# Optimization experiments

Measured on AMD Instinct MI355X. Metric: run time of the kernel, lower is better.

## Reference

```python
import jax, jax.numpy as jnp
import numpy as np

B, N, M, K = 4, 16384, 16384, 16   # batch, points, centers, neighbors
C, O, G = 64, 64, 8                # in_planes, out_planes, group


def setup_inputs() -> dict:
    key = jax.random.key(0)
    ks = jax.random.split(key, 16)
    r = lambda i, sh, s=1.0: jax.random.normal(ks[i], sh, jnp.float32) * s
    return dict(
        center_pos=r(0, (B, M, 3)),
        center_fea=r(1, (B, C, M)),
        pos=r(2, (B, N, 3)),
        fea=r(3, (B, C, N)),
        idx=jax.random.randint(ks[4], (B, M, K), 0, N, jnp.int32),
        # linear q/k/v
        Wq=r(5, (C, O), 0.05), bq=jnp.zeros((O,), jnp.float32),
        Wk=r(6, (C, O), 0.05), bk=jnp.zeros((O,), jnp.float32),
        Wv=r(7, (C, O), 0.05), bv=jnp.zeros((O,), jnp.float32),
        # center_pos_encode: conv1x1(3->O, no bias) + folded BN (scale,shift) + relu + conv1x1(O->O)
        cpe_w1=r(8, (3, O), 0.05), cpe_s=jnp.ones((O,), jnp.float32), cpe_b=jnp.zeros((O,), jnp.float32),
        cpe_w2=r(9, (O, O), 0.05), cpe_b2=jnp.zeros((O,), jnp.float32),
        # pos_encode (Conv2d 1x1 == per-point linear)
        pe_w1=r(10, (3, O), 0.05), pe_s=jnp.ones((O,), jnp.float32), pe_b=jnp.zeros((O,), jnp.float32),
        pe_w2=r(11, (O, O), 0.05), pe_b2=jnp.zeros((O,), jnp.float32),
        # weight_encode (O -> G)
        we_w1=r(12, (O, G), 0.05), we_s=jnp.ones((G,), jnp.float32), we_b=jnp.zeros((G,), jnp.float32),
        we_w2=r(13, (G, G), 0.05), we_b2=jnp.zeros((G,), jnp.float32),
    )


def _mlp2(x, w1, s, b, w2, b2):
    # conv1x1(no bias) -> inference BatchNorm folded to (scale, shift) -> ReLU -> conv1x1(+bias)
    h = jax.nn.relu(x @ w1 * s + b)
    return h @ w2 + b2


def reference(center_pos, center_fea, pos, fea, idx,
              Wq, bq, Wk, bk, Wv, bv,
              cpe_w1, cpe_s, cpe_b, cpe_w2, cpe_b2,
              pe_w1, pe_s, pe_b, pe_w2, pe_b2,
              we_w1, we_s, we_b, we_w2, we_b2):
    x_q = center_fea.transpose(0, 2, 1) @ Wq + bq        # [B,M,O]
    ft = fea.transpose(0, 2, 1)                          # [B,N,C]
    x_k = ft @ Wk + bk                                   # [B,N,O]
    x_v = ft @ Wv + bv                                   # [B,N,O]

    gather = jax.vmap(lambda a, i: a[i])                 # per-batch irregular gather
    nk = gather(x_k, idx)                                # [B,M,K,O]
    nv = gather(x_v, idx)                                # [B,M,K,O]
    npos = gather(pos, idx) - center_pos[:, :, None, :]  # [B,M,K,3] relative coords

    cpr = _mlp2(center_pos, cpe_w1, cpe_s, cpe_b, cpe_w2, cpe_b2)  # [B,M,O]
    pr = _mlp2(npos, pe_w1, pe_s, pe_b, pe_w2, pe_b2)              # [B,M,K,O]

    r_qk = nk - x_q[:, :, None, :] + cpr[:, :, None, :]  # [B,M,K,O]
    v = nv + pr                                          # [B,M,K,O]

    w = _mlp2(r_qk, we_w1, we_s, we_b, we_w2, we_b2)     # [B,M,K,G]
    w = jax.nn.softmax(w, axis=2)                        # softmax over neighbors

    v = v.reshape(B, M, K, G, O // G)
    out = jnp.einsum('bmkgi,bmkg->bmgi', v, w).reshape(B, M, O)
    return out.transpose(0, 2, 1)                        # [B,O,M]
```

## Files before the change

### kernel.cpp

```cpp
#include <hip/hip_runtime.h>
#include <hip/hip_bf16.h>

typedef unsigned short u16;
typedef __attribute__((ext_vector_type(8))) __bf16 bf8v;
typedef __attribute__((ext_vector_type(8))) _Float16 f16x8;
typedef __attribute__((ext_vector_type(2))) _Float16 h2v;
typedef __attribute__((ext_vector_type(4))) float f32x4;
typedef __attribute__((ext_vector_type(4))) unsigned uint4v;
typedef __attribute__((ext_vector_type(4))) int int4v;

#define B_ 4
#define N_ 16384
#define M_ 16384
#define K_ 16
#define C_ 64
#define O_ 64
#define G_ 8

__device__ __forceinline__ float bf2f(u16 x){
  union { unsigned u; float f; } v; v.u = ((unsigned)x) << 16; return v.f;
}
__device__ __forceinline__ u16 f2bf(float f){
  union { float f; unsigned u; } v; v.f = f;
  unsigned u = v.u;
  return (u16)((u + 0x7FFFu + ((u >> 16) & 1u)) >> 16);
}
__device__ __forceinline__ u16 f2h(float f){
  union { _Float16 h; u16 u; } v; v.h = (_Float16)f; return v.u;
}
__device__ __forceinline__ h2v mkh2(float a, float b){
  h2v r = {(_Float16)a, (_Float16)b}; return r;
}

__global__ __launch_bounds__(256) void pre_kernel(
    const float* __restrict__ center_pos, const float* __restrict__ center_fea,
    const float* __restrict__ pos, const float* __restrict__ fea,
    const float* __restrict__ Wq, const float* __restrict__ bq,
    const float* __restrict__ Wk, const float* __restrict__ bk,
    const float* __restrict__ Wv, const float* __restrict__ bv,
    const float* __restrict__ cpe_w1, const float* __restrict__ cpe_s, const float* __restrict__ cpe_b,
    const float* __restrict__ cpe_w2, const float* __restrict__ cpe_b2,
    const float* __restrict__ we_w1,
    u16* __restrict__ xk, u16* __restrict__ xv, float* __restrict__ qw,
    float* __restrict__ pos4, float* __restrict__ cp4)
{
  __shared__ u16 sWT[128*72];
  __shared__ u16 sA[64*72];
  __shared__ u16 sOut[64*136];
  __shared__ float sMisc[256];
  __shared__ float sCi[8];
  int tid = threadIdx.x;
  int l = tid & 63, w = tid >> 6, c = l & 15, q = l >> 4;
  int blk = blockIdx.x;

  if (blk < 256){
    int P0 = blk * 256; int b = P0 >> 14; int n00 = P0 & (N_-1);
    const float* fb = fea + (long)b*C_*N_;
    for (int e = tid; e < 8192; e += 256){
      int k = e >> 7, col = e & 127;
      float v = (col < 64) ? Wk[k*64 + col] : Wv[k*64 + (col-64)];
      sWT[col*72 + k] = f2bf(v);
    }
    if (tid < 128) sMisc[tid] = (tid < 64) ? bk[tid] : bv[tid-64];
    {
      long pg = (long)P0 + tid;
      f32x4 r = {pos[pg*3], pos[pg*3+1], pos[pg*3+2], 0.f};
      ((f32x4*)pos4)[pg] = r;
    }

    #pragma unroll 1
    for (int s = 0; s < 4; s++){
      int n0 = n00 + s*64;
      #pragma unroll
      for (int pp = 0; pp < 4; pp++){
        int k = pp*16 + (tid >> 4);
        int nf = (tid & 15)*4;
        f32x4 v = *(const f32x4*)&fb[(long)k*N_ + n0 + nf];
        sA[(nf+0)*72+k] = f2bf(v[0]); sA[(nf+1)*72+k] = f2bf(v[1]);
        sA[(nf+2)*72+k] = f2bf(v[2]); sA[(nf+3)*72+k] = f2bf(v[3]);
      }
      __syncthreads();

      bf8v af0 = *(const bf8v*)&sA[(w*16+c)*72 + q*8];
      bf8v af1 = *(const bf8v*)&sA[(w*16+c)*72 + 32 + q*8];
      f32x4 acc[8];
      #pragma unroll
      for (int t = 0; t < 8; t++){
        float bb = sMisc[16*t + c];
        f32x4 a_ = {bb, bb, bb, bb};
        bf8v b0 = *(const bf8v*)&sWT[(16*t + c)*72 + q*8];
        bf8v b1 = *(const bf8v*)&sWT[(16*t + c)*72 + 32 + q*8];
        a_ = __builtin_amdgcn_mfma_f32_16x16x32_bf16(af0, b0, a_, 0,0,0);
        a_ = __builtin_amdgcn_mfma_f32_16x16x32_bf16(af1, b1, a_, 0,0,0);
        acc[t] = a_;
      }
      #pragma unroll
      for (int t = 0; t < 8; t++)
        #pragma unroll
        for (int r = 0; r < 4; r++)
          sOut[(w*16 + q*4 + r)*136 + 16*t + c] = f2bf(acc[t][r]);
      __syncthreads();

      #pragma unroll
      for (int rep = 0; rep < 4; rep++){
        int chunk = rep*256 + tid;
        int pt = chunk >> 4, c8i = chunk & 15;
        uint4v val = *(const uint4v*)&sOut[pt*136 + c8i*8];
        int col8 = c8i*8;
        long row = (long)P0 + s*64 + pt;
        if (col8 < 64) *(uint4v*)(xk + row*64 + col8)      = val;
        else           *(uint4v*)(xv + row*64 + (col8-64)) = val;
      }
      __syncthreads();
    }
  } else {
    int P0 = (blk - 256) * 256; int b = P0 >> 14; int m00 = P0 & (M_-1);
    const float* cfb = center_fea + (long)b*C_*M_;
    float* sWe = (float*)sOut;
    float* sQ  = (float*)sOut;
    for (int e = tid; e < 512; e += 256) sWe[e] = we_w1[e];
    if (tid < 64){
      float sc = cpe_s[tid];
      sMisc[tid]     = cpe_w1[tid]*sc;
      sMisc[64+tid]  = cpe_w1[64+tid]*sc;
      sMisc[128+tid] = cpe_w1[128+tid]*sc;
      sMisc[192+tid] = cpe_b[tid];
    }
    {
      long pg = (long)P0 + tid;
      f32x4 r = {center_pos[pg*3], center_pos[pg*3+1], center_pos[pg*3+2], 0.f};
      ((f32x4*)cp4)[pg] = r;
    }
    __syncthreads();
    {
      int k = tid >> 1, g0 = (tid & 1)*4;
      const float* brow = (k < 64) ? (cpe_w2 + k*64) : (Wq + (k-64)*64);
      float sgn = (k < 64) ? 1.f : -1.f;
      float aw[4] = {0.f,0.f,0.f,0.f};
      for (int o = 0; o < 64; o++){
        float bo = brow[o]*sgn;
        #pragma unroll
        for (int gg=0; gg<4; gg++) aw[gg] += bo * sWe[o*8 + g0+gg];
      }
      #pragma unroll
      for (int gg=0; gg<4; gg++) sWT[(g0+gg)*136 + k] = f2bf(aw[gg]);
    }
    for (int e = tid; e < 2176; e += 256){
      int r = e / 136, cc = e % 136;
      if (r >= 8 || cc >= 128) sWT[e] = 0;
    }
    if (tid < 8){
      float s = 0.f;
      for (int o = 0; o < 64; o++) s += (cpe_b2[o] - bq[o]) * sWe[o*8 + tid];
      sCi[tid] = s;
    }
    __syncthreads();

    #pragma unroll 1
    for (int s = 0; s < 4; s++){
      int m0 = m00 + s*64;
      #pragma unroll
      for (int pp = 0; pp < 4; pp++){
        int k = pp*16 + (tid >> 4);
        int nf = (tid & 15)*4;
        f32x4 v = *(const f32x4*)&cfb[(long)k*M_ + m0 + nf];
        sA[(nf+0)*72+k] = f2bf(v[0]); sA[(nf+1)*72+k] = f2bf(v[1]);
        sA[(nf+2)*72+k] = f2bf(v[2]); sA[(nf+3)*72+k] = f2bf(v[3]);
      }
      long c3 = (long)(P0 + s*64 + w*16 + c)*3;
      float cp0 = center_pos[c3], cp1 = center_pos[c3+1], cp2 = center_pos[c3+2];
      __syncthreads();

      bf8v ah[2];
      #pragma unroll
      for (int ks = 0; ks < 2; ks++){
        union { bf8v v; u16 sv[8]; } ua;
        #pragma unroll
        for (int j = 0; j < 8; j++){
          int h = ks*32 + q*8 + j;
          float hv = cp0*sMisc[h] + cp1*sMisc[64+h] + cp2*sMisc[128+h] + sMisc[192+h];
          ua.sv[j] = f2bf(fmaxf(hv, 0.f));
        }
        ah[ks] = ua.v;
      }
      bf8v acf0 = *(const bf8v*)&sA[(w*16+c)*72 + q*8];
      bf8v acf1 = *(const bf8v*)&sA[(w*16+c)*72 + 32 + q*8];

      float ci = (c < 8) ? sCi[c] : 0.f;
      f32x4 aq = {ci, ci, ci, ci};
      {
        bf8v b0 = *(const bf8v*)&sWT[c*136 + q*8];
        bf8v b1 = *(const bf8v*)&sWT[c*136 + 32 + q*8];
        bf8v b2 = *(const bf8v*)&sWT[c*136 + 64 + q*8];
        bf8v b3 = *(const bf8v*)&sWT[c*136 + 96 + q*8];
        aq = __builtin_amdgcn_mfma_f32_16x16x32_bf16(ah[0], b0, aq, 0,0,0);
        aq = __builtin_amdgcn_mfma_f32_16x16x32_bf16(ah[1], b1, aq, 0,0,0);
        aq = __builtin_amdgcn_mfma_f32_16x16x32_bf16(acf0,  b2, aq, 0,0,0);
        aq = __builtin_amdgcn_mfma_f32_16x16x32_bf16(acf1,  b3, aq, 0,0,0);
      }
      __syncthreads();
      if (c < 8){
        #pragma unroll
        for (int r = 0; r < 4; r++) sQ[(w*16 + q*4 + r)*8 + c] = aq[r];
      }
      __syncthreads();
      for (int e = tid; e < 512; e += 256)
        qw[(long)(P0 + s*64)*8 + e] = sQ[e];
      __syncthreads();
    }
  }
}

__global__ __launch_bounds__(256) void attn_kernel(
    const float* __restrict__ cp4, const float* __restrict__ pos4,
    const int* __restrict__ idx,
    const float* __restrict__ pe_w1, const float* __restrict__ pe_s, const float* __restrict__ pe_b,
    const float* __restrict__ pe_w2, const float* __restrict__ pe_b2,
    const float* __restrict__ we_w1, const float* __restrict__ we_s, const float* __restrict__ we_b,
    const float* __restrict__ we_w2, const float* __restrict__ we_b2,
    const u16* __restrict__ xk, const u16* __restrict__ xv, const float* __restrict__ qw,
    float* __restrict__ out)
{
  int tid = threadIdx.x;
  __shared__ float s_w1f[192], s_pb[64], s_pb2[64], s_ww2[64];
  __shared__ float s_ws8[8], s_wb8[8], s_wb28[8];
  __shared__ f32x4 s_dyn4[720];
  __shared__ float s_tile[64*66];

  char* dynb = (char*)s_dyn4;

  if (tid < 64){
    float sc = pe_s[tid];
    s_w1f[tid]     = pe_w1[tid]*sc;
    s_w1f[64+tid]  = pe_w1[64+tid]*sc;
    s_w1f[128+tid] = pe_w1[128+tid]*sc;
    s_pb[tid]  = pe_b[tid];
    s_pb2[tid] = pe_b2[tid];
    s_ww2[tid] = we_w2[tid];
  }
  if (tid >= 64 && tid < 72){
    int g = tid-64;
    s_ws8[g]=we_s[g]; s_wb8[g]=we_b[g]; s_wb28[g]=we_b2[g];
  }
  u16* stg = (u16*)dynb;
  #pragma unroll
  for (int pp = 0; pp < 4; pp++){
    int row = pp*16 + (tid >> 4);
    int colf = (tid & 15)*4;
    f32x4 v = *(const f32x4*)&pe_w2[row*64 + colf];
    stg[(colf+0)*72+row] = f2h(v[0]); stg[(colf+1)*72+row] = f2h(v[1]);
    stg[(colf+2)*72+row] = f2h(v[2]); stg[(colf+3)*72+row] = f2h(v[3]);
  }
  u16* stg2 = (u16*)(dynb + 9216);
  for (int e = tid; e < 512; e += 256){
    int k = e >> 3, cc = e & 7;
    stg2[cc*72 + k] = f2bf(we_w1[e]);
  }
  for (int e = tid; e < 576; e += 256) stg2[576 + e] = 0;
  __syncthreads();

  int w = tid >> 6, l = tid & 63, c = l & 15, q = l >> 4, c8 = c & 7;

  f16x8 pw2f[4][2];
  bf8v ww1f[2];
  f16x8 w2B, hz8;
  #pragma unroll
  for (int t = 0; t < 4; t++){
    pw2f[t][0] = *(const f16x8*)&stg[(t*16+c)*72 + q*8];
    pw2f[t][1] = *(const f16x8*)&stg[(t*16+c)*72 + 32 + q*8];
  }
  ww1f[0] = *(const bf8v*)&stg2[c*72 + q*8];
  ww1f[1] = *(const bf8v*)&stg2[c*72 + 32 + q*8];
  {
    union { f16x8 v; u16 s[8]; } uu;
    #pragma unroll
    for (int j = 0; j < 8; j++)
      uu.s[j] = (q == 0 && c < 8) ? f2h(s_ww2[j*8 + c]) : (u16)0;
    w2B = uu.v;
    #pragma unroll
    for (int j = 0; j < 8; j++) uu.s[j] = 0;
    hz8 = uu.v;
  }
  h2v cw0[2][4], cw1[2][4], cw2[2][4], cb[2][4];
  #pragma unroll
  for (int ks = 0; ks < 2; ks++)
    #pragma unroll
    for (int jj = 0; jj < 4; jj++){
      int o = ks*32 + q*8 + jj*2;
      cw0[ks][jj] = mkh2(s_w1f[o],     s_w1f[o+1]);
      cw1[ks][jj] = mkh2(s_w1f[64+o],  s_w1f[65+o]);
      cw2[ks][jj] = mkh2(s_w1f[128+o], s_w1f[129+o]);
      cb [ks][jj] = mkh2(s_pb[o],      s_pb[o+1]);
    }
  int qok = (q < 2);
  int gq = (q & 1)*4;
  float wsr0 = qok ? s_ws8[gq+0] : 0.f, wbr0 = qok ? s_wb8[gq+0] : 0.f;
  float wsr1 = qok ? s_ws8[gq+1] : 0.f, wbr1 = qok ? s_wb8[gq+1] : 0.f;
  float wsr2 = qok ? s_ws8[gq+2] : 0.f, wbr2 = qok ? s_wb8[gq+2] : 0.f;
  float wsr3 = qok ? s_ws8[gq+3] : 0.f, wbr3 = qok ? s_wb8[gq+3] : 0.f;
  float wb2_c = s_wb28[c8];
  float pb2l = s_pb2[l];
  h2v hz2 = {(_Float16)0.f, (_Float16)0.f};
  __syncthreads();

  float* swt0 = (float*)(dynb + w*1536);
  float* swt1 = swt0 + 192;

  int blk = blockIdx.x;
  int pbase = (((blk & 7) << 7) | (blk >> 3)) * 64;
  int b = pbase >> 14;
  const u16* xkb = xk + (long)b * N_ * 64;
  const u16* xvb = xv + (long)b * N_ * 64;
  const f32x4* pos4b = ((const f32x4*)pos4) + (long)b * N_;
  int ch = c >> 3;

  int pb0 = pbase + w*16;
  const int*   idxl = idx + (long)pb0*16 + c;
  const int*   idxq = idx + (long)pb0*16 + q*4;
  const f32x4* qwl4 = ((const f32x4*)(qw + (long)pb0*8)) + (q & 1);
  const f32x4* cp4l = ((const f32x4*)cp4) + pb0;

  auto hidden_sm = [&](bf8v k0, bf8v k1, f32x4 qv, float* swtp){
    f32x4 h2t = {qv[0], qv[1], qv[2], qv[3]};
    h2t = __builtin_amdgcn_mfma_f32_16x16x32_bf16(ww1f[0], k0, h2t, 0,0,0);
    h2t = __builtin_amdgcn_mfma_f32_16x16x32_bf16(ww1f[1], k1, h2t, 0,0,0);
    h2v hp01 = mkh2(fmaxf(h2t[0]*wsr0 + wbr0, 0.f), fmaxf(h2t[1]*wsr1 + wbr1, 0.f));
    h2v hp23 = mkh2(fmaxf(h2t[2]*wsr2 + wbr2, 0.f), fmaxf(h2t[3]*wsr3 + wbr3, 0.f));
    union { h2v h; int i; } u01, u23, x01, x23;
    u01.h = hp01; u23.h = hp23;
    x01.i = __shfl_xor(u01.i, 16, 64);
    x23.i = __shfl_xor(u23.i, 16, 64);
    f16x8 ahf;
    {
      union { f16x8 v; h2v p[4]; } au;
      au.p[0] = u01.h; au.p[1] = u23.h; au.p[2] = x01.h; au.p[3] = x23.h;
      ahf = (q == 0) ? au.v : hz8;
    }
    f32x4 wlv = {wb2_c, wb2_c, wb2_c, wb2_c};
    wlv = __builtin_amdgcn_mfma_f32_16x16x32_f16(ahf, w2B, wlv, 0,0,0);
    float e0 = exp2f(wlv[0]*1.44269504f);
    float e1 = exp2f(wlv[1]*1.44269504f);
    float e2 = exp2f(wlv[2]*1.44269504f);
    float e3 = exp2f(wlv[3]*1.44269504f);
    float sm = e0+e1+e2+e3;
    sm += __shfl_xor(sm, 16, 64);
    sm += __shfl_xor(sm, 32, 64);
    float rn = 1.0f / sm;
    if (c < 8){
      f32x4 ev = {e0*rn, e1*rn, e2*rn, e3*rn};
      *(f32x4*)&swtp[c*20 + q*4] = ev;
    }
  };

  struct H1 { f16x8 a, b; };
  auto make_h1 = [&](float n0, float n1, float n2){
    h2v n0h = {(_Float16)n0, (_Float16)n0};
    h2v n1h = {(_Float16)n1, (_Float16)n1};
    h2v n2h = {(_Float16)n2, (_Float16)n2};
    H1 o;
    #pragma unroll
    for (int ks = 0; ks < 2; ks++){
      union { f16x8 v; h2v p[4]; } hu;
      #pragma unroll
      for (int jj = 0; jj < 4; jj++){
        h2v a = cb[ks][jj];
        a = n0h*cw0[ks][jj] + a;
        a = n1h*cw1[ks][jj] + a;
        a = n2h*cw2[ks][jj] + a;
        hu.p[jj] = __builtin_elementwise_max(a, hz2);
      }
      if (ks == 0) o.a = hu.v; else o.b = hu.v;
    }
    return o;
  };

  auto finish = [&](H1 h, unsigned (&vv)[4][4],
                    f32x4 wv0, f32x4 wv1, f32x4 wv2, f32x4 wv3, int row){
    float ov[4];
    #pragma unroll
    for (int t = 0; t < 4; t++){
      f32x4 z = {bf2f((u16)vv[0][t]), bf2f((u16)vv[1][t]),
                 bf2f((u16)vv[2][t]), bf2f((u16)vv[3][t])};
      z = __builtin_amdgcn_mfma_f32_16x16x32_f16(h.a, pw2f[t][0], z, 0,0,0);
      z = __builtin_amdgcn_mfma_f32_16x16x32_f16(h.b, pw2f[t][1], z, 0,0,0);
      f32x4 wv = (t==0) ? wv0 : (t==1) ? wv1 : (t==2) ? wv2 : wv3;
      ov[t] = z[0]*wv[0] + z[1]*wv[1] + z[2]*wv[2] + z[3]*wv[3];
    }
    int hi2 = (q & 2);
    float s0 = hi2 ? ov[0] : ov[2];
    float s1 = hi2 ? ov[1] : ov[3];
    float m0 = hi2 ? ov[2] : ov[0];
    float m1 = hi2 ? ov[3] : ov[1];
    float u_ = m0 + __shfl_xor(s0, 32, 64);
    float v_ = m1 + __shfl_xor(s1, 32, 64);
    float s2 = (q & 1) ? u_ : v_;
    float m2 = (q & 1) ? v_ : u_;
    float ovsel = m2 + __shfl_xor(s2, 16, 64);
    s_tile[row*66 + l] = ovsel + pb2l;
  };

  int j0 = idxl[0];
  int j1 = idxl[16];
  int ivE = idxl[32];
  int ivO = idxl[48];
  f32x4 qvP = qwl4[0];
  f32x4 qvO = qwl4[2];
  f32x4 qvE = qwl4[4];
  f32x4 cpE = cp4l[0], cpO = cp4l[1];
  f32x4 ppE = pos4b[j0], ppO = pos4b[j1];
  const u16* krP = xkb + (size_t)j0*64;
  bf8v kP0 = *(const bf8v*)(krP + q*8);
  bf8v kP1 = *(const bf8v*)(krP + 32 + q*8);
  const u16* kr1 = xkb + (size_t)j1*64;
  bf8v kO0 = *(const bf8v*)(kr1 + q*8);
  bf8v kO1 = *(const bf8v*)(kr1 + 32 + q*8);
  int4v iq0 = *(const int4v*)&idxq[0];
  int4v iqO = *(const int4v*)&idxq[16];
  int4v iqE = *(const int4v*)&idxq[32];
  unsigned vcE[4][4];
  #pragma unroll
  for (int r = 0; r < 4; r++){
    const u16* vr = xvb + (size_t)iq0[r]*64 + c;
    #pragma unroll
    for (int t = 0; t < 4; t++) vcE[r][t] = vr[t*16];
  }
  hidden_sm(kP0, kP1, qvP, swt0);

  #pragma unroll 1
  for (int ii = 0; ii < 8; ii++){
    int i0 = 2*ii, i1 = i0 + 1;

    f32x4 wa0 = *(const f32x4*)&swt0[(0*2+ch)*20 + q*4];
    f32x4 wa1 = *(const f32x4*)&swt0[(1*2+ch)*20 + q*4];
    f32x4 wa2 = *(const f32x4*)&swt0[(2*2+ch)*20 + q*4];
    f32x4 wa3 = *(const f32x4*)&swt0[(3*2+ch)*20 + q*4];
    float na0 = ppE[0]-cpE[0], na1 = ppE[1]-cpE[1], na2 = ppE[2]-cpE[2];
    const u16* krE = xkb + (size_t)ivE*64;
    bf8v kE20 = *(const bf8v*)(krE + q*8);
    bf8v kE21 = *(const bf8v*)(krE + 32 + q*8);
    ppE = pos4b[ivE];
    cpE = cp4l[(i0+2 <= 15) ? i0+2 : 15];
    unsigned vcO[4][4];
    #pragma unroll
    for (int r = 0; r < 4; r++){
      const u16* vr = xvb + (size_t)iqO[r]*64 + c;
      #pragma unroll
      for (int t = 0; t < 4; t++) vcO[r][t] = vr[t*16];
    }
    iqO = *(const int4v*)&idxq[((i0+3 <= 15) ? i0+3 : 15)*16];
    ivE = idxl[((i0+4 <= 15) ? i0+4 : 15)*16];
    hidden_sm(kO0, kO1, qvO, swt1);
    qvO = qwl4[((i0+3 <= 15) ? i0+3 : 15)*2];
    H1 hE = make_h1(na0, na1, na2);
    finish(hE, vcE, wa0, wa1, wa2, wa3, w*16 + i0);

    f32x4 wb0 = *(const f32x4*)&swt1[(0*2+ch)*20 + q*4];
    f32x4 wb1 = *(const f32x4*)&swt1[(1*2+ch)*20 + q*4];
    f32x4 wb2 = *(const f32x4*)&swt1[(2*2+ch)*20 + q*4];
    f32x4 wb3 = *(const f32x4*)&swt1[(3*2+ch)*20 + q*4];
    float nb0 = ppO[0]-cpO[0], nb1 = ppO[1]-cpO[1], nb2 = ppO[2]-cpO[2];
    const u16* krO = xkb + (size_t)ivO*64;
    kO0 = *(const bf8v*)(krO + q*8);
    kO1 = *(const bf8v*)(krO + 32 + q*8);
    ppO = pos4b[ivO];
    cpO = cp4l[(i0+3 <= 15) ? i0+3 : 15];
    #pragma unroll
    for (int r = 0; r < 4; r++){
      const u16* vr = xvb + (size_t)iqE[r]*64 + c;
      #pragma unroll
      for (int t = 0; t < 4; t++) vcE[r][t] = vr[t*16];
    }
    iqE = *(const int4v*)&idxq[((i0+4 <= 15) ? i0+4 : 15)*16];
    ivO = idxl[((i0+5 <= 15) ? i0+5 : 15)*16];
    if (ii < 7)
      hidden_sm(kE20, kE21, qvE, swt0);
    qvE = qwl4[((i0+4 <= 15) ? i0+4 : 15)*2];
    H1 hO = make_h1(nb0, nb1, nb2);
    finish(hO, vcO, wb0, wb1, wb2, wb3, w*16 + i1);
  }
  __syncthreads();

  {
    int o0 = tid >> 5, pt0 = tid & 31;
    int m0 = pbase & (M_-1);
    #pragma unroll
    for (int half = 0; half < 2; half++){
      int pt = pt0 + half*32;
      long outb = ((long)b*64) * M_ + m0 + pt;
      #pragma unroll
      for (int ii = 0; ii < 8; ii++){
        int o = o0*8 + ii;
        out[outb + (long)o*M_] = s_tile[pt*66 + o];
      }
    }
  }
}

extern "C" void kernel_launch(void* const* d_in, const int* in_sizes, int n_in,
                              void* d_out, int out_size, void* d_ws, size_t ws_size,
                              hipStream_t stream) {
  const float* center_pos = (const float*)d_in[0];
  const float* center_fea = (const float*)d_in[1];
  const float* pos        = (const float*)d_in[2];
  const float* fea        = (const float*)d_in[3];
  const int*   idx        = (const int*)d_in[4];
  const float* Wq = (const float*)d_in[5];   const float* bq = (const float*)d_in[6];
  const float* Wk = (const float*)d_in[7];   const float* bk = (const float*)d_in[8];
  const float* Wv = (const float*)d_in[9];   const float* bv = (const float*)d_in[10];
  const float* cpe_w1 = (const float*)d_in[11]; const float* cpe_s = (const float*)d_in[12];
  const float* cpe_b  = (const float*)d_in[13]; const float* cpe_w2 = (const float*)d_in[14];
  const float* cpe_b2 = (const float*)d_in[15];
  const float* pe_w1 = (const float*)d_in[16]; const float* pe_s = (const float*)d_in[17];
  const float* pe_b  = (const float*)d_in[18]; const float* pe_w2 = (const float*)d_in[19];
  const float* pe_b2 = (const float*)d_in[20];
  const float* we_w1 = (const float*)d_in[21]; const float* we_s = (const float*)d_in[22];
  const float* we_b  = (const float*)d_in[23]; const float* we_w2 = (const float*)d_in[24];
  const float* we_b2 = (const float*)d_in[25];

  const size_t SZ = (size_t)B_*N_*64;
  u16* xk = (u16*)d_ws;
  u16* xv = xk + SZ;
  float* qwp = (float*)(xv + SZ);
  float* pos4p = qwp + (size_t)B_*M_*8;
  float* cp4p  = pos4p + (size_t)B_*N_*4;
  float* outp = (float*)d_out;

  hipLaunchKernelGGL(pre_kernel, dim3(512), dim3(256), 0, stream,
      center_pos, center_fea, pos, fea, Wq, bq, Wk, bk, Wv, bv,
      cpe_w1, cpe_s, cpe_b, cpe_w2, cpe_b2, we_w1,
      xk, xv, qwp, pos4p, cp4p);
  hipLaunchKernelGGL(attn_kernel, dim3(1024), dim3(256), 0, stream,
      cp4p, pos4p, idx, pe_w1, pe_s, pe_b, pe_w2, pe_b2,
      we_w1, we_s, we_b, we_w2, we_b2, xk, xv, qwp, outp);
}
```

Baseline: 188.8 us.

## Double-buffer feature tiles in pre_kernel to prefetch next tile during MFMA

Adds a second shared-memory staging buffer and issues the global loads for the next 64-point tile before the current tile's MFMA work, writing them to the alternate buffer afterwards. It also removes one barrier in the query branch. This is meant to hide global load latency behind compute in the pre-pass. The cost is extra LDS and registers, which may lower occupancy. The pre-kernel is likely a small part of total time next to the attention kernel.

```diff
diff --git a/kernel.cpp b/kernel.cpp
--- a/kernel.cpp
+++ b/kernel.cpp
@@ -45,13 +45,15 @@
     float* __restrict__ pos4, float* __restrict__ cp4)
 {
   __shared__ u16 sWT[128*72];
-  __shared__ u16 sA[64*72];
+  __shared__ u16 sA0[64*72];
+  __shared__ u16 sA1[64*72];
   __shared__ u16 sOut[64*136];
   __shared__ float sMisc[256];
   __shared__ float sCi[8];
   int tid = threadIdx.x;
   int l = tid & 63, w = tid >> 6, c = l & 15, q = l >> 4;
   int blk = blockIdx.x;
+  int kk = tid >> 4, nf = (tid & 15)*4;
 
   if (blk < 256){
     int P0 = blk * 256; int b = P0 >> 14; int n00 = P0 & (N_-1);
@@ -67,22 +69,29 @@
       f32x4 r = {pos[pg*3], pos[pg*3+1], pos[pg*3+2], 0.f};
       ((f32x4*)pos4)[pg] = r;
     }
+    #pragma unroll
+    for (int pp = 0; pp < 4; pp++){
+      int k = pp*16 + kk;
+      f32x4 v = *(const f32x4*)&fb[(long)k*N_ + n00 + nf];
+      sA0[(nf+0)*72+k] = f2bf(v[0]); sA0[(nf+1)*72+k] = f2bf(v[1]);
+      sA0[(nf+2)*72+k] = f2bf(v[2]); sA0[(nf+3)*72+k] = f2bf(v[3]);
+    }
+    __syncthreads();
 
     #pragma unroll 1
     for (int s = 0; s < 4; s++){
-      int n0 = n00 + s*64;
-      #pragma unroll
-      for (int pp = 0; pp < 4; pp++){
-        int k = pp*16 + (tid >> 4);
-        int nf = (tid & 15)*4;
-        f32x4 v = *(const f32x4*)&fb[(long)k*N_ + n0 + nf];
-        sA[(nf+0)*72+k] = f2bf(v[0]); sA[(nf+1)*72+k] = f2bf(v[1]);
-        sA[(nf+2)*72+k] = f2bf(v[2]); sA[(nf+3)*72+k] = f2bf(v[3]);
-      }
-      __syncthreads();
-
-      bf8v af0 = *(const bf8v*)&sA[(w*16+c)*72 + q*8];
-      bf8v af1 = *(const bf8v*)&sA[(w*16+c)*72 + 32 + q*8];
+      u16* curA = (s & 1) ? sA1 : sA0;
+      u16* nxtA = (s & 1) ? sA0 : sA1;
+      f32x4 ld0, ld1, ld2, ld3;
+      if (s < 3){
+        int n1 = n00 + (s+1)*64;
+        ld0 = *(const f32x4*)&fb[(long)( 0+kk)*N_ + n1 + nf];
+        ld1 = *(const f32x4*)&fb[(long)(16+kk)*N_ + n1 + nf];
+        ld2 = *(const f32x4*)&fb[(long)(32+kk)*N_ + n1 + nf];
+        ld3 = *(const f32x4*)&fb[(long)(48+kk)*N_ + n1 + nf];
+      }
+      bf8v af0 = *(const bf8v*)&curA[(w*16+c)*72 + q*8];
+      bf8v af1 = *(const bf8v*)&curA[(w*16+c)*72 + 32 + q*8];
       f32x4 acc[8];
       #pragma unroll
       for (int t = 0; t < 8; t++){
@@ -99,6 +108,16 @@
         #pragma unroll
         for (int r = 0; r < 4; r++)
           sOut[(w*16 + q*4 + r)*136 + 16*t + c] = f2bf(acc[t][r]);
+      if (s < 3){
+        nxtA[(nf+0)*72 + ( 0+kk)] = f2bf(ld0[0]); nxtA[(nf+1)*72 + ( 0+kk)] = f2bf(ld0[1]);
+        nxtA[(nf+2)*72 + ( 0+kk)] = f2bf(ld0[2]); nxtA[(nf+3)*72 + ( 0+kk)] = f2bf(ld0[3]);
+        nxtA[(nf+0)*72 + (16+kk)] = f2bf(ld1[0]); nxtA[(nf+1)*72 + (16+kk)] = f2bf(ld1[1]);
+        nxtA[(nf+2)*72 + (16+kk)] = f2bf(ld1[2]); nxtA[(nf+3)*72 + (16+kk)] = f2bf(ld1[3]);
+        nxtA[(nf+0)*72 + (32+kk)] = f2bf(ld2[0]); nxtA[(nf+1)*72 + (32+kk)] = f2bf(ld2[1]);
+        nxtA[(nf+2)*72 + (32+kk)] = f2bf(ld2[2]); nxtA[(nf+3)*72 + (32+kk)] = f2bf(ld2[3]);
+        nxtA[(nf+0)*72 + (48+kk)] = f2bf(ld3[0]); nxtA[(nf+1)*72 + (48+kk)] = f2bf(ld3[1]);
+        nxtA[(nf+2)*72 + (48+kk)] = f2bf(ld3[2]); nxtA[(nf+3)*72 + (48+kk)] = f2bf(ld3[3]);
+      }
       __syncthreads();
 
       #pragma unroll
@@ -154,22 +173,29 @@
       for (int o = 0; o < 64; o++) s += (cpe_b2[o] - bq[o]) * sWe[o*8 + tid];
       sCi[tid] = s;
     }
+    #pragma unroll
+    for (int pp = 0; pp < 4; pp++){
+      int k = pp*16 + kk;
+      f32x4 v = *(const f32x4*)&cfb[(long)k*M_ + m00 + nf];
+      sA0[(nf+0)*72+k] = f2bf(v[0]); sA0[(nf+1)*72+k] = f2bf(v[1]);
+      sA0[(nf+2)*72+k] = f2bf(v[2]); sA0[(nf+3)*72+k] = f2bf(v[3]);
+    }
     __syncthreads();
 
     #pragma unroll 1
     for (int s = 0; s < 4; s++){
-      int m0 = m00 + s*64;
-      #pragma unroll
-      for (int pp = 0; pp < 4; pp++){
-        int k = pp*16 + (tid >> 4);
-        int nf = (tid & 15)*4;
-        f32x4 v = *(const f32x4*)&cfb[(long)k*M_ + m0 + nf];
-        sA[(nf+0)*72+k] = f2bf(v[0]); sA[(nf+1)*72+k] = f2bf(v[1]);
-        sA[(nf+2)*72+k] = f2bf(v[2]); sA[(nf+3)*72+k] = f2bf(v[3]);
+      u16* curA = (s & 1) ? sA1 : sA0;
+      u16* nxtA = (s & 1) ? sA0 : sA1;
+      f32x4 ld0, ld1, ld2, ld3;
+      if (s < 3){
+        int m1 = m00 + (s+1)*64;
+        ld0 = *(const f32x4*)&cfb[(long)( 0+kk)*M_ + m1 + nf];
+        ld1 = *(const f32x4*)&cfb[(long)(16+kk)*M_ + m1 + nf];
+        ld2 = *(const f32x4*)&cfb[(long)(32+kk)*M_ + m1 + nf];
+        ld3 = *(const f32x4*)&cfb[(long)(48+kk)*M_ + m1 + nf];
       }
       long c3 = (long)(P0 + s*64 + w*16 + c)*3;
       float cp0 = center_pos[c3], cp1 = center_pos[c3+1], cp2 = center_pos[c3+2];
-      __syncthreads();
 
       bf8v ah[2];
       #pragma unroll
@@ -183,8 +209,8 @@
         }
         ah[ks] = ua.v;
       }
-      bf8v acf0 = *(const bf8v*)&sA[(w*16+c)*72 + q*8];
-      bf8v acf1 = *(const bf8v*)&sA[(w*16+c)*72 + 32 + q*8];
+      bf8v acf0 = *(const bf8v*)&curA[(w*16+c)*72 + q*8];
+      bf8v acf1 = *(const bf8v*)&curA[(w*16+c)*72 + 32 + q*8];
 
       float ci = (c < 8) ? sCi[c] : 0.f;
       f32x4 aq = {ci, ci, ci, ci};
@@ -198,7 +224,16 @@
         aq = __builtin_amdgcn_mfma_f32_16x16x32_bf16(acf0,  b2, aq, 0,0,0);
         aq = __builtin_amdgcn_mfma_f32_16x16x32_bf16(acf1,  b3, aq, 0,0,0);
       }
-      __syncthreads();
+      if (s < 3){
+        nxtA[(nf+0)*72 + ( 0+kk)] = f2bf(ld0[0]); nxtA[(nf+1)*72 + ( 0+kk)] = f2bf(ld0[1]);
+        nxtA[(nf+2)*72 + ( 0+kk)] = f2bf(ld0[2]); nxtA[(nf+3)*72 + ( 0+kk)] = f2bf(ld0[3]);
+        nxtA[(nf+0)*72 + (16+kk)] = f2bf(ld1[0]); nxtA[(nf+1)*72 + (16+kk)] = f2bf(ld1[1]);
+        nxtA[(nf+2)*72 + (16+kk)] = f2bf(ld1[2]); nxtA[(nf+3)*72 + (16+kk)] = f2bf(ld1[3]);
+        nxtA[(nf+0)*72 + (32+kk)] = f2bf(ld2[0]); nxtA[(nf+1)*72 + (32+kk)] = f2bf(ld2[1]);
+        nxtA[(nf+2)*72 + (32+kk)] = f2bf(ld2[2]); nxtA[(nf+3)*72 + (32+kk)] = f2bf(ld2[3]);
+        nxtA[(nf+0)*72 + (48+kk)] = f2bf(ld3[0]); nxtA[(nf+1)*72 + (48+kk)] = f2bf(ld3[1]);
+        nxtA[(nf+2)*72 + (48+kk)] = f2bf(ld3[2]); nxtA[(nf+3)*72 + (48+kk)] = f2bf(ld3[3]);
+      }
       if (c < 8){
         #pragma unroll
         for (int r = 0; r < 4; r++) sQ[(w*16 + q*4 + r)*8 + c] = aq[r];
```

After: 190.5 us. About the same (+0.9%).
